# Performance work log

Measured on AMD Instinct MI355X. Metric: run time of the kernel, lower is better.

The kernel has to match this reference:

```python
import jax, jax.numpy as jnp
import numpy as np

N_QUBITS = 10
BATCH = 16384
Q_DEPTH = 2


def _apply_1q_shared(state, U, q):
    # state: [B, 2, 2, ..., 2]; U: [2, 2] complex, acting on wire q
    state = jnp.moveaxis(state, 1 + q, -1)
    state = jnp.einsum('b...i,ji->b...j', state, U)
    return jnp.moveaxis(state, -1, 1 + q)


def _apply_ry_batched(state, angles, q):
    # per-sample RY(angle) on wire q; angles: [B] float
    c = jnp.cos(angles * 0.5).astype(jnp.complex64)
    s = jnp.sin(angles * 0.5).astype(jnp.complex64)
    U = jnp.stack([jnp.stack([c, -s], -1), jnp.stack([s, c], -1)], -2)  # [B,2,2]
    state = jnp.moveaxis(state, 1 + q, -1)
    state = jnp.einsum('b...i,bji->b...j', state, U)
    return jnp.moveaxis(state, -1, 1 + q)


def _rot_matrix(phi, theta, omega):
    # PennyLane Rot = RZ(omega) @ RY(theta) @ RZ(phi)
    c = jnp.cos(theta * 0.5)
    s = jnp.sin(theta * 0.5)
    m00 = jnp.exp(-0.5j * (phi + omega)) * c
    m01 = -jnp.exp(0.5j * (phi - omega)) * s
    m10 = jnp.exp(-0.5j * (phi - omega)) * s
    m11 = jnp.exp(0.5j * (phi + omega)) * c
    return jnp.stack([jnp.stack([m00, m01]), jnp.stack([m10, m11])]).astype(jnp.complex64)


def _apply_cnot(state, c, t):
    st = jnp.moveaxis(state, (1 + c, 1 + t), (1, 2))  # [B, ctrl, tgt, ...]
    st = jnp.stack([st[:, 0], st[:, 1, ::-1]], axis=1)  # flip target where ctrl=1
    return jnp.moveaxis(st, (1, 2), (1 + c, 1 + t))


def setup_inputs() -> dict:
    key = jax.random.key(0)
    k1, k2 = jax.random.split(key)
    x = jax.random.uniform(k1, (BATCH, N_QUBITS), dtype=jnp.float32) * np.pi
    q_weights = 0.01 * jax.random.normal(k2, (Q_DEPTH, N_QUBITS, 3), dtype=jnp.float32)
    return {"x": x, "q_weights": q_weights}


def reference(x, q_weights) -> jnp.ndarray:
    B, n = x.shape
    L = q_weights.shape[0]
    # |0...0> statevector, batched: [B] + [2]*n (axis q <-> wire q, wire 0 most significant)
    state = jnp.zeros((B, 2 ** n), jnp.complex64).at[:, 0].set(1.0)
    state = state.reshape((B,) + (2,) * n)
    # AngleEmbedding(rotation='Y')
    for q in range(n):
        state = _apply_ry_batched(state, x[:, q], q)
    # StronglyEntanglingLayers: Rot on each wire, then ring of CNOTs with range (l % (n-1)) + 1
    for l in range(L):
        for q in range(n):
            U = _rot_matrix(q_weights[l, q, 0], q_weights[l, q, 1], q_weights[l, q, 2])
            state = _apply_1q_shared(state, U, q)
        r = (l % (n - 1)) + 1
        for q in range(n):
            state = _apply_cnot(state, q, (q + r) % n)
    probs = jnp.abs(state.reshape(B, 2 ** n)) ** 2  # [B, 2^n]
    bits = (np.arange(2 ** n)[:, None] >> (n - 1 - np.arange(n))[None, :]) & 1
    signs = jnp.asarray(1.0 - 2.0 * bits, jnp.float32)  # [2^n, n], PauliZ eigenvalues
    return (probs @ signs).astype(jnp.float32)  # [B, n] expvals
```

## Files before the change

### kernel.cpp

```cpp
#include <hip/hip_runtime.h>

#define DEVINL __device__ __forceinline__

typedef float f32x2 __attribute__((ext_vector_type(2)));

struct GC { int laneXor, regXor, rowL, rowR; };
struct Circ { GC g[20]; int sgnL[10], sgnR[10]; int lsel[5]; };

constexpr Circ build_circ() {
    Circ c{};
    unsigned A[10] = {};
    for (int i = 0; i < 10; ++i) A[i] = 1u << i;
    for (int w = 0; w < 10; ++w) {
        int pos = 9 - w;
        unsigned m = 1u << pos;
        c.g[w] = GC{ int(m >> 5), int(m & 31u), int(m >> 5), int(m & 31u) };
    }
    for (int q = 0; q < 10; ++q) { int pc = 9 - q, pt = 9 - ((q + 1) % 10); A[pt] ^= A[pc]; }
    unsigned M[10] = {}, Inv[10] = {};
    for (int i = 0; i < 10; ++i) { M[i] = A[i]; Inv[i] = 1u << i; }
    for (int col = 0; col < 10; ++col) {
        int piv = col;
        while (!((M[piv] >> col) & 1u)) ++piv;
        unsigned tm = M[col]; M[col] = M[piv]; M[piv] = tm;
        unsigned ti = Inv[col]; Inv[col] = Inv[piv]; Inv[piv] = ti;
        for (int r = 0; r < 10; ++r)
            if (r != col && ((M[r] >> col) & 1u)) { M[r] ^= M[col]; Inv[r] ^= Inv[col]; }
    }
    for (int w = 0; w < 10; ++w) {
        int pos = 9 - w;
        unsigned m = 0;
        for (int i = 0; i < 10; ++i) m |= ((Inv[i] >> pos) & 1u) << i;
        unsigned row = A[pos];
        c.g[10 + w] = GC{ int(m >> 5), int(m & 31u), int(row >> 5), int(row & 31u) };
    }
    for (int q = 0; q < 10; ++q) { int pc = 9 - q, pt = 9 - ((q + 2) % 10); A[pt] ^= A[pc]; }
    for (int q = 0; q < 10; ++q) { unsigned row = A[9 - q]; c.sgnL[q] = int(row >> 5); c.sgnR[q] = int(row & 31u); }

    unsigned Ucols[5] = {};
    {
        unsigned tgt[5] = {16, 8, 7, 2, 1};
        unsigned acc = 0;
        for (int k = 0; k < 5; ++k) { acc ^= tgt[k]; Ucols[k] = acc; }
    }
    unsigned Urows[5] = {};
    for (int r = 0; r < 5; ++r)
        for (int cc = 0; cc < 5; ++cc)
            Urows[r] |= ((Ucols[cc] >> r) & 1u) << cc;
    unsigned MM[5] = {}, AI[5] = {};
    for (int i = 0; i < 5; ++i) { MM[i] = Urows[i]; AI[i] = 1u << i; }
    for (int col = 0; col < 5; ++col) {
        int piv = col;
        while (!((MM[piv] >> col) & 1u)) ++piv;
        unsigned tm = MM[col]; MM[col] = MM[piv]; MM[piv] = tm;
        unsigned ti = AI[col]; AI[col] = AI[piv]; AI[piv] = ti;
        for (int r = 0; r < 5; ++r)
            if (r != col && ((MM[r] >> col) & 1u)) { MM[r] ^= MM[col]; AI[r] ^= AI[col]; }
    }
    for (int w = 0; w < 10; ++w) {
        unsigned mL = unsigned(c.g[10 + w].laneXor);
        unsigned nm = 0;
        for (int i = 0; i < 5; ++i) if ((mL >> i) & 1u) nm ^= Ucols[i];
        c.g[10 + w].laneXor = int(nm);
        unsigned rL = unsigned(c.g[10 + w].rowL);
        unsigned nr = 0;
        for (int i = 0; i < 5; ++i) if ((rL >> i) & 1u) nr ^= AI[i];
        c.g[10 + w].rowL = int(nr);
    }
    for (int q = 0; q < 10; ++q) {
        unsigned sL = unsigned(c.sgnL[q]);
        unsigned ns = 0;
        for (int i = 0; i < 5; ++i) if ((sL >> i) & 1u) ns ^= AI[i];
        c.sgnL[q] = int(ns);
    }
    for (int o = 0; o < 5; ++o) c.lsel[o] = int(AI[o]);
    return c;
}

constexpr Circ CC = build_circ();

static_assert(CC.g[10].laneXor == 1  && CC.g[10].regXor == 0,  "w0");
static_assert(CC.g[11].laneXor == 2  && CC.g[11].regXor == 0,  "w1");
static_assert(CC.g[12].laneXor == 7  && CC.g[12].regXor == 0,  "w2");
static_assert(CC.g[13].laneXor == 8  && CC.g[13].regXor == 0,  "w3");
static_assert(CC.g[14].laneXor == 16 && CC.g[14].regXor == 16, "w4");
static_assert(CC.g[15].laneXor == 0  && CC.g[15].regXor == 24, "w5");
static_assert(CC.g[16].laneXor == 0  && CC.g[16].regXor == 12, "w6");
static_assert(CC.g[17].laneXor == 0  && CC.g[17].regXor == 6,  "w7");
static_assert(CC.g[18].laneXor == 0  && CC.g[18].regXor == 3,  "w8");
static_assert(CC.g[19].laneXor == 1  && CC.g[19].regXor == 1,  "w9");
static_assert(CC.g[10].rowR == 31, "w0 rowR");
static_assert(CC.g[11].rowR == 0,  "w1 rowR");
static_assert(CC.g[12].rowR == 0,  "w2 rowR");
static_assert(CC.g[13].rowR == 0,  "w3 rowR");
static_assert(CC.g[14].rowR == 0,  "w4 rowR");
static_assert(CC.g[15].rowR == 16, "w5 rowR");
static_assert(CC.g[16].rowR == 24, "w6 rowR");
static_assert(CC.g[17].rowR == 28, "w7 rowR");
static_assert(CC.g[18].rowR == 30, "w8 rowR");
static_assert(CC.g[19].rowR == 31, "w9 rowR");

DEVINL float csw(float v, int sw) {
    return __int_as_float(__float_as_int(v) ^ sw);
}

template<int XOR>
DEVINL float fetch(float v, int lane) {
    if constexpr (XOR == 0)      return v;
    else if constexpr (XOR == 1) return __int_as_float(__builtin_amdgcn_update_dpp(0, __float_as_int(v), 0xB1, 0xF, 0xF, true));
    else if constexpr (XOR == 2) return __int_as_float(__builtin_amdgcn_update_dpp(0, __float_as_int(v), 0x4E, 0xF, 0xF, true));
    else if constexpr (XOR == 3) return __int_as_float(__builtin_amdgcn_update_dpp(0, __float_as_int(v), 0x1B, 0xF, 0xF, true));
    else if constexpr (XOR == 7) return __int_as_float(__builtin_amdgcn_update_dpp(0, __float_as_int(v), 0x141, 0xF, 0xF, true));
    else if constexpr (XOR == 8) return __int_as_float(__builtin_amdgcn_update_dpp(0, __float_as_int(v), 0x128, 0xF, 0xF, true));
    else                         return __int_as_float(__builtin_amdgcn_ds_swizzle(__float_as_int(v), 0x1F | (XOR << 10)));
}

DEVINL void pk_fma_acc(f32x2& a, f32x2 t, f32x2 b) {
    asm("v_pk_fma_f32 %0, %1, %2, %0" : "+v"(a) : "v"(t), "v"(b));
}

DEVINL f32x2 cmul(f32x2 a, f32x2 b) {
    f32x2 r;
    r.x = a.x * b.x - a.y * b.y;
    r.y = a.x * b.y + a.y * b.x;
    return r;
}

__device__ __attribute__((aligned(16))) float g_cst[80];

__global__ void qprep(const float* __restrict__ qw) {
    int g = threadIdx.x;
    if (g < 10) {
        float phi = qw[g * 3 + 0], th = qw[g * 3 + 1], om = qw[g * 3 + 2];
        float c = cosf(0.5f * th), s = sinf(0.5f * th);
        float apo = 0.5f * (phi + om), amo = 0.5f * (phi - om);
        g_cst[g * 4 + 0] =  cosf(apo) * c;
        g_cst[g * 4 + 1] = -sinf(apo) * c;
        g_cst[g * 4 + 2] = -cosf(amo) * s;
        g_cst[g * 4 + 3] = -sinf(amo) * s;
    } else if (g < 20) {
        int w = g - 10;
        float phi = qw[g * 3 + 0], th = qw[g * 3 + 1];
        float c = cosf(0.5f * th), s = sinf(0.5f * th);
        g_cst[40 + w] = s / c;
        g_cst[50 + w * 2 + 0] =  cosf(0.5f * phi);
        g_cst[50 + w * 2 + 1] = -sinf(0.5f * phi);
    } else if (g == 20) {
        float p = 1.f;
        for (int w = 0; w < 10; ++w) p *= cosf(0.5f * qw[(10 + w) * 3 + 1]);
        g_cst[70] = p;
    }
}

DEVINL void wf(const float* cst, float xw, int w, f32x2& f0, f32x2& f1) {
    float h = 0.5f * xw;
    float s = __sinf(h), c = __cosf(h);
    float m0 = cst[w * 4 + 0], m1 = cst[w * 4 + 1], m2 = cst[w * 4 + 2], m3 = cst[w * 4 + 3];
    f0.x =  m0 * c + m2 * s;
    f0.y =  m1 * c + m3 * s;
    f1.x = -m2 * c + m0 * s;
    f1.y =  m3 * c - m1 * s;
}

template<int W>
DEVINL void apply_gate(f32x2 (&a2)[32], const float* cst, int lane, const int (&sw)[10]) {
    constexpr GC gc = CC.g[10 + W];
    float tt = csw(cst[40 + W], sw[W]);
    f32x2 tp; tp.x = tt;  tp.y = tt;
    f32x2 tn; tn.x = -tt; tn.y = -tt;
    if constexpr (gc.laneXor == 0) {
        #pragma unroll
        for (int r = 0; r < 32; ++r) {
            const int r2 = r ^ gc.regXor;
            if (r < r2) {
                f32x2 old = a2[r];
                const bool sR  = __builtin_popcount(unsigned(gc.rowR & r )) & 1;
                const bool sR2 = __builtin_popcount(unsigned(gc.rowR & r2)) & 1;
                pk_fma_acc(a2[r],  sR  ? tp : tn, a2[r2]);
                pk_fma_acc(a2[r2], sR2 ? tp : tn, old);
            }
        }
    } else {
        #pragma unroll
        for (int c = 0; c < 2; ++c) {
            f32x2 b2[16];
            #pragma unroll
            for (int i = 0; i < 16; ++i) {
                const int r = (i & 7) + c * 8 + ((i >> 3) << 4);
                f32x2 s = a2[r ^ gc.regXor];
                b2[i].x = fetch<gc.laneXor>(s.x, lane);
                b2[i].y = fetch<gc.laneXor>(s.y, lane);
            }
            #pragma unroll
            for (int i = 0; i < 16; ++i) {
                const int r = (i & 7) + c * 8 + ((i >> 3) << 4);
                const bool sR = __builtin_popcount(unsigned(gc.rowR & r)) & 1;
                pk_fma_acc(a2[r], sR ? tp : tn, b2[i]);
            }
        }
    }
}

__global__ __launch_bounds__(256) void qsim(const float* __restrict__ x,
                                            float* __restrict__ out, int B) {
    const float* cst = g_cst;
    int lane = threadIdx.x & 63;
    int l5 = lane & 31;
    int b = blockIdx.x * 8 + (threadIdx.x >> 5);
    if (b >= B) return;
    const float* xb = x + b * 10;

    int sw_[10];
    #pragma unroll
    for (int w = 0; w < 10; ++w)
        sw_[w] = (__popc(unsigned(l5 & CC.g[10 + w].rowL)) & 1) << 31;

    f32x2 t01[4], t23[4], f5t[2];
    {
        f32x2 a0, a1, b0, b1;
        wf(cst, xb[9], 9, a0, a1);
        wf(cst, xb[8], 8, b0, b1);
        t01[0] = cmul(a0, b0); t01[1] = cmul(a1, b0);
        t01[2] = cmul(a0, b1); t01[3] = cmul(a1, b1);
        wf(cst, xb[7], 7, a0, a1);
        wf(cst, xb[6], 6, b0, b1);
        t23[0] = cmul(a0, b0); t23[1] = cmul(a1, b0);
        t23[2] = cmul(a0, b1); t23[3] = cmul(a1, b1);
        wf(cst, xb[5], 5, f5t[0], f5t[1]);
    }

    f32x2 E0; E0.x = cst[50];      E0.y = csw(cst[51], sw_[0]);
    f32x2 E1; E1.x = cst[52];      E1.y = csw(cst[53], sw_[1]);
    f32x2 E2; E2.x = cst[54];      E2.y = csw(cst[55], sw_[2]);
    f32x2 E3; E3.x = cst[56];      E3.y = csw(cst[57], sw_[3]);
    f32x2 E4; E4.x = cst[58];      E4.y = csw(cst[59], sw_[4]);
    f32x2 E5; E5.x = cst[60];      E5.y = csw(cst[61], sw_[5]);
    f32x2 E6; E6.x = cst[62];      E6.y = csw(cst[63], sw_[6]);
    f32x2 E7; E7.x = cst[64];      E7.y = csw(cst[65], sw_[7]);
    f32x2 E8; E8.x = cst[66];      E8.y = csw(cst[67], sw_[8]);
    f32x2 E9; E9.x = cst[68];      E9.y = csw(cst[69], sw_[9]);

    f32x2 lf;
    {
        f32x2 ea = cmul(cmul(E1, E2), cmul(E3, E4));
        float sc = cst[70];
        lf.x = ea.x * sc; lf.y = ea.y * sc;
        #pragma unroll
        for (int jj = 0; jj < 5; ++jj) {
            int w = 4 - jj;
            f32x2 f0, f1;
            wf(cst, xb[w], w, f0, f1);
            int bit = __popc(unsigned(l5 & CC.lsel[jj])) & 1;
            f32x2 p; p.x = bit ? f1.x : f0.x; p.y = bit ? f1.y : f0.y;
            lf = cmul(lf, p);
        }
    }

    f32x2 f5p[2];
    f5p[0] = cmul(f5t[0], E5);
    { f32x2 e5c; e5c.x = E5.x; e5c.y = -E5.y; f5p[1] = cmul(f5t[1], e5c); }
    f32x2 V00 = cmul(E6, E7);
    f32x2 V01; { f32x2 e7c; e7c.x = E7.x; e7c.y = -E7.y; V01 = cmul(E6, e7c); }
    f32x2 EB = cmul(E9, E0);
    f32x2 H0 = cmul(E8, EB);
    f32x2 H1; { f32x2 ebc; ebc.x = EB.x; ebc.y = -EB.y; H1 = cmul(E8, ebc); }

    f32x2 tf[8];
    #pragma unroll
    for (int j = 0; j < 8; ++j) {
        f32x2 tA = cmul(t23[j & 3], f5p[j >> 2]);
        const int s6 = ((j >> 2) ^ (j >> 1)) & 1;
        const int s7 = s6 ^ (j & 1);
        f32x2 V;
        V.x = s6 ? (s7 ? V00.x : V01.x) : (s7 ? V01.x : V00.x);
        V.y = s6 ? -(s7 ? V00.y : V01.y) : (s7 ? V01.y : V00.y);
        tf[j] = cmul(tA, V);
    }

    f32x2 g4[4];
    #pragma unroll
    for (int v = 0; v < 4; ++v) g4[v] = cmul(lf, t01[v]);
    f32x2 a2[32];
    #pragma unroll
    for (int r = 0; r < 32; ++r) {
        f32x2 t = cmul(g4[r & 3], tf[(r >> 2) & 7]);
        f32x2 G;
        G.x = (r & 1) ? H1.x : H0.x;
        G.y = (r & 1) ? H1.y : H0.y;
        if (__builtin_popcount(unsigned(r & 30)) & 1) G.y = -G.y;
        a2[r] = cmul(t, G);
    }

    apply_gate<4>(a2, cst, lane, sw_);
    apply_gate<5>(a2, cst, lane, sw_);
    apply_gate<0>(a2, cst, lane, sw_);
    apply_gate<6>(a2, cst, lane, sw_);
    apply_gate<1>(a2, cst, lane, sw_);
    apply_gate<7>(a2, cst, lane, sw_);
    apply_gate<2>(a2, cst, lane, sw_);
    apply_gate<8>(a2, cst, lane, sw_);
    apply_gate<3>(a2, cst, lane, sw_);
    apply_gate<9>(a2, cst, lane, sw_);

    float wv[32];
    #pragma unroll
    for (int r = 0; r < 32; ++r) wv[r] = a2[r].x * a2[r].x + a2[r].y * a2[r].y;
    #pragma unroll
    for (int bS = 1; bS < 16; bS <<= 1) {
        #pragma unroll
        for (int r = 0; r < 32; ++r) {
            if (!(r & bS)) {
                float xv = wv[r], yv = wv[r | bS];
                wv[r]      = xv + yv;
                wv[r | bS] = xv - yv;
            }
        }
    }

    float e[10];
    #pragma unroll
    for (int q = 0; q < 10; ++q) {
        const int R = CC.sgnR[q];
        float num = (R & 16) ? (wv[R ^ 16] - wv[R]) : (wv[R] + wv[R ^ 16]);
        int slq = __popc(unsigned(l5 & CC.sgnL[q])) & 1;
        e[q] = csw(num, slq << 31);
    }

    #pragma unroll
    for (int q = 0; q < 10; ++q) {
        e[q] += fetch<1>(e[q], lane);
        e[q] += fetch<2>(e[q], lane);
    }
    int s = l5 & 3;
    bool s1 = (s & 1) != 0, s2 = (s & 2) != 0;
    float v0 = s1 ? e[1] : e[0];
    float u0 = s1 ? e[3] : e[2];
    v0 = s2 ? u0 : v0;
    float v1 = s1 ? e[5] : e[4];
    float u1 = s1 ? e[7] : e[6];
    v1 = s2 ? u1 : v1;
    float v2 = s1 ? e[9] : e[8];

    v0 += fetch<4>(v0, lane);   v1 += fetch<4>(v1, lane);   v2 += fetch<4>(v2, lane);
    v0 += fetch<8>(v0, lane);   v1 += fetch<8>(v1, lane);   v2 += fetch<8>(v2, lane);
    v0 += fetch<16>(v0, lane);  v1 += fetch<16>(v1, lane);  v2 += fetch<16>(v2, lane);

    float vo = v0;
    int hi = l5 >> 2;
    vo = (hi == 1) ? v1 : vo;
    vo = (hi == 2) ? v2 : vo;
    if (l5 < 10) out[b * 10 + l5] = vo;
}

extern "C" void kernel_launch(void* const* d_in, const int* in_sizes, int n_in,
                              void* d_out, int out_size, void* d_ws, size_t ws_size,
                              hipStream_t stream) {
    const float* x  = (const float*)d_in[0];
    const float* qw = (const float*)d_in[1];
    float* out = (float*)d_out;
    int B = in_sizes[0] / 10;
    int blocks = (B + 7) / 8;
    hipLaunchKernelGGL(qprep, dim3(1), dim3(64), 0, stream, qw);
    hipLaunchKernelGGL(qsim, dim3(blocks), dim3(256), 0, stream, x, out, B);
}
```

Before: 84.56 us.

## Remap lane basis, specialize lane-only gates, vectorize input loads, restructure init products

Changes the lane-bit basis choice so that wire 2's gate uses a lane xor of 2 instead of 7, and reorders the final gate sequence. Adds a specialized path for gates that only shuffle across lanes, and rewrites the mixed lane/register path to fetch per register pair. Loads the per-sample input as five float2 vector loads, and restructures the initial product tree to shorten dependency chains. Together these aim to cut cross-lane shuffle cost and initialization latency. The risk is higher register pressure and possible ordering errors if the gate reordering is not valid.

```diff
diff --git a/kernel.cpp b/kernel.cpp
--- a/kernel.cpp
+++ b/kernel.cpp
@@ -39,7 +39,7 @@
 
     unsigned Ucols[5] = {};
     {
-        unsigned tgt[5] = {16, 8, 7, 2, 1};
+        unsigned tgt[5] = {16, 8, 2, 12, 1};
         unsigned acc = 0;
         for (int k = 0; k < 5; ++k) { acc ^= tgt[k]; Ucols[k] = acc; }
     }
@@ -80,8 +80,8 @@
 constexpr Circ CC = build_circ();
 
 static_assert(CC.g[10].laneXor == 1  && CC.g[10].regXor == 0,  "w0");
-static_assert(CC.g[11].laneXor == 2  && CC.g[11].regXor == 0,  "w1");
-static_assert(CC.g[12].laneXor == 7  && CC.g[12].regXor == 0,  "w2");
+static_assert(CC.g[11].laneXor == 12 && CC.g[11].regXor == 0,  "w1");
+static_assert(CC.g[12].laneXor == 2  && CC.g[12].regXor == 0,  "w2");
 static_assert(CC.g[13].laneXor == 8  && CC.g[13].regXor == 0,  "w3");
 static_assert(CC.g[14].laneXor == 16 && CC.g[14].regXor == 16, "w4");
 static_assert(CC.g[15].laneXor == 0  && CC.g[15].regXor == 24, "w5");
@@ -180,22 +180,29 @@
                 pk_fma_acc(a2[r2], sR2 ? tp : tn, old);
             }
         }
+    } else if constexpr (gc.regXor == 0) {
+        #pragma unroll
+        for (int r = 0; r < 32; ++r) {
+            f32x2 b;
+            b.x = fetch<gc.laneXor>(a2[r].x, lane);
+            b.y = fetch<gc.laneXor>(a2[r].y, lane);
+            const bool sR = __builtin_popcount(unsigned(gc.rowR & r)) & 1;
+            pk_fma_acc(a2[r], sR ? tp : tn, b);
+        }
     } else {
         #pragma unroll
-        for (int c = 0; c < 2; ++c) {
-            f32x2 b2[16];
-            #pragma unroll
-            for (int i = 0; i < 16; ++i) {
-                const int r = (i & 7) + c * 8 + ((i >> 3) << 4);
-                f32x2 s = a2[r ^ gc.regXor];
-                b2[i].x = fetch<gc.laneXor>(s.x, lane);
-                b2[i].y = fetch<gc.laneXor>(s.y, lane);
-            }
-            #pragma unroll
-            for (int i = 0; i < 16; ++i) {
-                const int r = (i & 7) + c * 8 + ((i >> 3) << 4);
-                const bool sR = __builtin_popcount(unsigned(gc.rowR & r)) & 1;
-                pk_fma_acc(a2[r], sR ? tp : tn, b2[i]);
+        for (int r = 0; r < 32; ++r) {
+            const int r2 = r ^ gc.regXor;
+            if (r < r2) {
+                f32x2 blo, bhi;
+                blo.x = fetch<gc.laneXor>(a2[r2].x, lane);
+                blo.y = fetch<gc.laneXor>(a2[r2].y, lane);
+                bhi.x = fetch<gc.laneXor>(a2[r].x, lane);
+                bhi.y = fetch<gc.laneXor>(a2[r].y, lane);
+                const bool sR  = __builtin_popcount(unsigned(gc.rowR & r )) & 1;
+                const bool sR2 = __builtin_popcount(unsigned(gc.rowR & r2)) & 1;
+                pk_fma_acc(a2[r],  sR  ? tp : tn, blo);
+                pk_fma_acc(a2[r2], sR2 ? tp : tn, bhi);
             }
         }
     }
@@ -208,7 +215,11 @@
     int l5 = lane & 31;
     int b = blockIdx.x * 8 + (threadIdx.x >> 5);
     if (b >= B) return;
-    const float* xb = x + b * 10;
+
+    const f32x2* xp = reinterpret_cast<const f32x2*>(x + b * 10);
+    f32x2 xv0 = xp[0], xv1 = xp[1], xv2 = xp[2], xv3 = xp[3], xv4 = xp[4];
+    float xw[10] = { xv0.x, xv0.y, xv1.x, xv1.y, xv2.x,
+                     xv2.y, xv3.x, xv3.y, xv4.x, xv4.y };
 
     int sw_[10];
     #pragma unroll
@@ -218,15 +229,15 @@
     f32x2 t01[4], t23[4], f5t[2];
     {
         f32x2 a0, a1, b0, b1;
-        wf(cst, xb[9], 9, a0, a1);
-        wf(cst, xb[8], 8, b0, b1);
+        wf(cst, xw[9], 9, a0, a1);
+        wf(cst, xw[8], 8, b0, b1);
         t01[0] = cmul(a0, b0); t01[1] = cmul(a1, b0);
         t01[2] = cmul(a0, b1); t01[3] = cmul(a1, b1);
-        wf(cst, xb[7], 7, a0, a1);
-        wf(cst, xb[6], 6, b0, b1);
+        wf(cst, xw[7], 7, a0, a1);
+        wf(cst, xw[6], 6, b0, b1);
         t23[0] = cmul(a0, b0); t23[1] = cmul(a1, b0);
         t23[2] = cmul(a0, b1); t23[3] = cmul(a1, b1);
-        wf(cst, xb[5], 5, f5t[0], f5t[1]);
+        wf(cst, xw[5], 5, f5t[0], f5t[1]);
     }
 
     f32x2 E0; E0.x = cst[50];      E0.y = csw(cst[51], sw_[0]);
@@ -242,18 +253,22 @@
 
     f32x2 lf;
     {
-        f32x2 ea = cmul(cmul(E1, E2), cmul(E3, E4));
-        float sc = cst[70];
-        lf.x = ea.x * sc; lf.y = ea.y * sc;
+        f32x2 p[5];
         #pragma unroll
         for (int jj = 0; jj < 5; ++jj) {
             int w = 4 - jj;
             f32x2 f0, f1;
-            wf(cst, xb[w], w, f0, f1);
+            wf(cst, xw[w], w, f0, f1);
             int bit = __popc(unsigned(l5 & CC.lsel[jj])) & 1;
-            f32x2 p; p.x = bit ? f1.x : f0.x; p.y = bit ? f1.y : f0.y;
-            lf = cmul(lf, p);
-        }
+            p[jj].x = bit ? f1.x : f0.x;
+            p[jj].y = bit ? f1.y : f0.y;
+        }
+        f32x2 ea = cmul(cmul(E1, E2), cmul(E3, E4));
+        float sc = cst[70];
+        ea.x *= sc; ea.y *= sc;
+        f32x2 q01 = cmul(p[0], p[1]);
+        f32x2 q23 = cmul(p[2], p[3]);
+        lf = cmul(cmul(q01, q23), cmul(ea, p[4]));
     }
 
     f32x2 f5p[2];
@@ -277,29 +292,32 @@
         tf[j] = cmul(tA, V);
     }
 
-    f32x2 g4[4];
-    #pragma unroll
-    for (int v = 0; v < 4; ++v) g4[v] = cmul(lf, t01[v]);
+    f32x2 g4H[4][2];
+    #pragma unroll
+    for (int v = 0; v < 4; ++v) {
+        f32x2 g = cmul(lf, t01[v]);
+        f32x2 H = (v & 1) ? H1 : H0;
+        g4H[v][0] = cmul(g, H);
+        f32x2 Hc; Hc.x = H.x; Hc.y = -H.y;
+        g4H[v][1] = cmul(g, Hc);
+    }
     f32x2 a2[32];
     #pragma unroll
     for (int r = 0; r < 32; ++r) {
-        f32x2 t = cmul(g4[r & 3], tf[(r >> 2) & 7]);
-        f32x2 G;
-        G.x = (r & 1) ? H1.x : H0.x;
-        G.y = (r & 1) ? H1.y : H0.y;
-        if (__builtin_popcount(unsigned(r & 30)) & 1) G.y = -G.y;
-        a2[r] = cmul(t, G);
+        const int v = r & 3, j = (r >> 2) & 7;
+        const int sel = ((v >> 1) ^ __builtin_popcount(unsigned(j))) & 1;
+        a2[r] = cmul(g4H[v][sel], tf[j]);
     }
 
     apply_gate<4>(a2, cst, lane, sw_);
     apply_gate<5>(a2, cst, lane, sw_);
-    apply_gate<0>(a2, cst, lane, sw_);
+    apply_gate<3>(a2, cst, lane, sw_);
     apply_gate<6>(a2, cst, lane, sw_);
     apply_gate<1>(a2, cst, lane, sw_);
     apply_gate<7>(a2, cst, lane, sw_);
     apply_gate<2>(a2, cst, lane, sw_);
     apply_gate<8>(a2, cst, lane, sw_);
-    apply_gate<3>(a2, cst, lane, sw_);
+    apply_gate<0>(a2, cst, lane, sw_);
     apply_gate<9>(a2, cst, lane, sw_);
 
     float wv[32];
@@ -310,9 +328,9 @@
         #pragma unroll
         for (int r = 0; r < 32; ++r) {
             if (!(r & bS)) {
-                float xv = wv[r], yv = wv[r | bS];
-                wv[r]      = xv + yv;
-                wv[r | bS] = xv - yv;
+                float xvv = wv[r], yv = wv[r | bS];
+                wv[r]      = xvv + yv;
+                wv[r | bS] = xvv - yv;
             }
         }
     }
```

New measurement: 83.06 us. Within noise of the previous version (-1.8%).
